# Kernel optimization log

Measured on AMD Instinct MI355X. Metric: run time of the kernel, lower is better.

## Reference

```python
import jax, jax.numpy as jnp
import numpy as np

N, C_IN, C_OUT, T, V = 64, 128, 128, 128, 25
REL = C_IN // 8  # rel_channels = 16


def setup_inputs() -> dict:
    key = jax.random.key(0)
    ks = jax.random.split(key, 12)
    s_in = 1.0 / np.sqrt(C_IN)
    s_rel = 1.0 / np.sqrt(REL)
    return {
        "x": jax.random.normal(ks[0], (N, C_IN, T, V), jnp.float32),
        "A": jax.random.normal(ks[1], (V, V), jnp.float32),
        "alpha": jnp.float32(1.0),
        "W1": jax.random.normal(ks[2], (REL, C_IN), jnp.float32) * s_in,
        "b1": jnp.zeros((REL,), jnp.float32),
        "W2": jax.random.normal(ks[3], (REL, C_IN), jnp.float32) * s_in,
        "b2": jnp.zeros((REL,), jnp.float32),
        "W3": jax.random.normal(ks[4], (C_OUT, C_IN), jnp.float32) * s_in,
        "b3": jnp.zeros((C_OUT,), jnp.float32),
        "W4": jax.random.normal(ks[5], (C_OUT, REL), jnp.float32) * s_rel,
        "b4": jnp.zeros((C_OUT,), jnp.float32),
    }


def reference(x, A, alpha, W1, b1, W2, b2, W3, b3, W4, b4):
    # conv1(x).mean(-2) and conv2(x).mean(-2): 1x1 conv is linear, so mean over
    # T commutes with it -> compute mean first to avoid an (N,REL,T,V) temp.
    xm = x.mean(axis=2)                                        # (N, C, V)
    x1 = jnp.einsum('rc,ncv->nrv', W1, xm) + b1[None, :, None]  # (N, R, V)
    x2 = jnp.einsum('rc,ncv->nrv', W2, xm) + b2[None, :, None]  # (N, R, V)
    x3 = jnp.einsum('oc,nctv->notv', W3, x) + b3[None, :, None, None]  # (N,O,T,V)
    # tanh of broadcasted pairwise difference: (N, R, V, V)
    d = jnp.tanh(x1[:, :, :, None] - x2[:, :, None, :])
    # conv4 (1x1 over channel dim) -> learned per-channel adjacency
    adj = jnp.einsum('or,nrvu->novu', W4, d) + b4[None, :, None, None]
    adj = adj * alpha + A[None, None, :, :]                    # (N, O, V, V)
    return jnp.einsum('ncvu,nctv->nctu', adj, x3)              # (N, O, T, V)
```

## Files before the change

### kernel.cpp

```cpp
#include <hip/hip_runtime.h>


#define NB   64
#define CIN  128
#define COUT 128
#define TT   128
#define VV   25
#define REL  16

#define JT 25
#define KT 4
#define CT 8
#define XF_BYTES (JT * KT * 1024)
#define W3F_OFF  XF_BYTES
#define LDS_BYTES (XF_BYTES + CT * KT * 1024)
#define X3_STRIDE 1040

typedef __attribute__((ext_vector_type(8))) short bf16x8;
typedef __attribute__((ext_vector_type(4))) float f32x4;

__device__ inline short f2bf(float f) {
    unsigned u = __float_as_uint(f);
    u += 0x7fff + ((u >> 16) & 1);
    return (short)(u >> 16);
}

__launch_bounds__(256)
__global__ void k_mean(const float* __restrict__ x, float* __restrict__ xm) {
    __shared__ float tile[4 * 3200];
    int tid = threadIdx.x;
    int c0 = blockIdx.x * 4, n = blockIdx.y;
    const float* src = x + ((size_t)n * CIN + c0) * 3200;
    for (int i = tid; i < 3200; i += 256)
        *reinterpret_cast<float4*>(&tile[i * 4]) =
            *reinterpret_cast<const float4*>(src + (size_t)i * 4);
    __syncthreads();
    if (tid < 100) {
        int cl = tid / 25, v = tid - cl * 25;
        const float* r = &tile[cl * 3200 + v];
        float s = 0.f;
#pragma unroll
        for (int t = 0; t < TT; ++t) s += r[t * 25];
        xm[((size_t)n * CIN + c0 + cl) * 25 + v] = s * (1.0f / TT);
    }
}

__global__ void k_adj(const float* __restrict__ xm,
                      const float* __restrict__ A, const float* __restrict__ alphap,
                      const float* __restrict__ W1, const float* __restrict__ b1,
                      const float* __restrict__ W2, const float* __restrict__ b2,
                      const float* __restrict__ W4, const float* __restrict__ b4,
                      char* __restrict__ adjT) {
    __shared__ char adjS[32 * 2048];
    __shared__ float xms[CIN * VV];
    __shared__ float W1s[REL * CIN];
    __shared__ float W2s[REL * CIN];
    __shared__ float x1s[REL * VV];
    __shared__ float x2s[REL * VV];
    __shared__ float W4s[32 * REL];
    __shared__ float b4s[32];

    int tid = threadIdx.x;
    int n = blockIdx.x;
    int o0 = blockIdx.y * 32;

    for (int i = tid; i < 16384; i += 256) reinterpret_cast<float*>(adjS)[i] = 0.f;
    for (int i = tid; i < CIN * VV; i += 256) xms[i] = xm[(size_t)n * CIN * VV + i];
    for (int i = tid; i < REL * CIN; i += 256) { W1s[i] = W1[i]; W2s[i] = W2[i]; }
    for (int i = tid; i < 32 * REL; i += 256) W4s[i] = W4[o0 * REL + i];
    if (tid < 32) b4s[tid] = b4[o0 + tid];
    __syncthreads();

    for (int task = tid; task < 2 * REL * VV; task += 256) {
        int rv = task % (REL * VV);
        int which = task / (REL * VV);
        int r = rv / VV, v = rv % VV;
        const float* Ws = which ? W2s : W1s;
        float s = 0.f;
#pragma unroll 8
        for (int c = 0; c < CIN; ++c) s = fmaf(Ws[r * CIN + c], xms[c * VV + v], s);
        s += which ? b2[r] : b1[r];
        (which ? x2s : x1s)[rv] = s;
    }
    __syncthreads();

    float alpha = alphap[0];
    for (int p = tid; p < VV * VV; p += 256) {
        int v = p / VV, u = p % VV;
        float d[REL];
#pragma unroll
        for (int r = 0; r < REL; ++r) d[r] = tanhf(x1s[r * VV + v] - x2s[r * VV + u]);
        float Avu = A[v * VV + u];
        int off = (u >> 4) * 1024 + (((u & 15) + 16 * (v >> 3)) * 16) + (v & 7) * 2;
        for (int oo = 0; oo < 32; ++oo) {
            float s = 0.f;
#pragma unroll
            for (int r = 0; r < REL; ++r) s = fmaf(W4s[oo * REL + r], d[r], s);
            float val = alpha * (s + b4s[oo]) + Avu;
            *(short*)(adjS + oo * 2048 + off) = f2bf(val);
        }
    }
    __syncthreads();

    float4* dst = reinterpret_cast<float4*>(adjT + (size_t)(n * COUT + o0) * 2048);
    const float4* src = reinterpret_cast<const float4*>(adjS);
    for (int i = tid; i < 4096; i += 256) dst[i] = src[i];
}

__launch_bounds__(512)
__global__ void k_main(const float* __restrict__ x, const float* __restrict__ W3,
                       const float* __restrict__ b3, const char* __restrict__ adjT,
                       float* __restrict__ out) {
    __shared__ __align__(16) char lds[LDS_BYTES];

    int tid = threadIdx.x;
    int tb = blockIdx.x, n = blockIdx.y;
    int lane = tid & 63, w = tid >> 6;
    int g = lane >> 4, lr = lane & 15;

    const float* xb = x + (size_t)n * (CIN * TT * VV) + tb * (16 * VV);

    bf16x8 xr[13];
#pragma unroll
    for (int q = 0; q < 13; ++q) {
        int chunk = tid + q * 512;
        if (chunk < JT * KT * 64) {
            int l = chunk & 63;
            int frag = chunk >> 6;
            int kt = frag / JT, jt = frag % JT;
            int j = jt * 16 + (l & 15);
            int kb = kt * 32 + 8 * (l >> 4);
            const float* p = xb + (size_t)kb * (TT * VV) + j;
#pragma unroll
            for (int b = 0; b < 8; ++b) xr[q][b] = f2bf(p[(size_t)b * (TT * VV)]);
        }
    }
#pragma unroll
    for (int q = 0; q < 13; ++q) {
        int chunk = tid + q * 512;
        if (chunk < JT * KT * 64)
            *reinterpret_cast<bf16x8*>(lds + (size_t)chunk * 16) = xr[q];
    }
#pragma unroll
    for (int q = 0; q < 4; ++q) {
        int chunk = tid + q * 512;
        int l = chunk & 63;
        int frag = chunk >> 6;
        int ct = frag >> 2, kt = frag & 3;
        int c = ct * 16 + (l & 15);
        int kb = kt * 32 + 8 * (l >> 4);
        const float4 f0 = *reinterpret_cast<const float4*>(&W3[(size_t)c * CIN + kb]);
        const float4 f1 = *reinterpret_cast<const float4*>(&W3[(size_t)c * CIN + kb + 4]);
        bf16x8 vv;
        vv[0] = f2bf(f0.x); vv[1] = f2bf(f0.y); vv[2] = f2bf(f0.z); vv[3] = f2bf(f0.w);
        vv[4] = f2bf(f1.x); vv[5] = f2bf(f1.y); vv[6] = f2bf(f1.z); vv[7] = f2bf(f1.w);
        *reinterpret_cast<bf16x8*>(lds + W3F_OFF + (size_t)chunk * 16) = vv;
    }
    __syncthreads();

    f32x4 acc[JT];
#pragma unroll
    for (int jt = 0; jt < JT; ++jt) acc[jt] = f32x4{0.f, 0.f, 0.f, 0.f};
#pragma unroll
    for (int kt = 0; kt < KT; ++kt) {
        bf16x8 a = *reinterpret_cast<const bf16x8*>(lds + W3F_OFF + ((w * 4 + kt) * 64 + lane) * 16);
#pragma unroll
        for (int jt = 0; jt < JT; ++jt) {
            bf16x8 bx = *reinterpret_cast<const bf16x8*>(lds + ((kt * JT + jt) * 64 + lane) * 16);
            acc[jt] = __builtin_amdgcn_mfma_f32_16x16x32_bf16(a, bx, acc[jt], 0, 0, 0);
        }
    }
    __syncthreads();

    int cbase = w * 16 + 4 * g;
    float bv[4];
#pragma unroll
    for (int r = 0; r < 4; ++r) bv[r] = b3[cbase + r];
#pragma unroll
    for (int jt = 0; jt < JT; ++jt) {
        int j = jt * 16 + lr;
        int t = j / 25, v = j - t * 25;
        int off = (t + 16 * (v >> 3)) * 16 + (v & 7) * 2;
#pragma unroll
        for (int r = 0; r < 4; ++r) {
            float val = acc[jt][r] + bv[r];
            *(short*)(lds + (size_t)(cbase + r) * X3_STRIDE + off) = f2bf(val);
        }
    }
    for (int z = lane; z < 16 * 16 * 7; z += 64) {
        int c = 16 * w + z / 112;
        int rem = z % 112;
        int t = rem / 7, qq = rem % 7;
        *(short*)(lds + (size_t)c * X3_STRIDE + (t + 48) * 16 + 2 + qq * 2) = 0;
    }

    const char* adjTb = adjT + (size_t)(n * COUT) * 2048;
    int t0 = tb * 16;
    for (int cc = 0; cc < 16; ++cc) {
        int c = w * 16 + cc;
        bf16x8 a = *reinterpret_cast<const bf16x8*>(lds + (size_t)c * X3_STRIDE + lane * 16);
        const bf16x8* bp = reinterpret_cast<const bf16x8*>(adjTb + (size_t)c * 2048);
        bf16x8 b0 = bp[lane];
        bf16x8 b1 = bp[64 + lane];
        f32x4 z = {0.f, 0.f, 0.f, 0.f};
        f32x4 d0 = __builtin_amdgcn_mfma_f32_16x16x32_bf16(a, b0, z, 0, 0, 0);
        f32x4 d1 = __builtin_amdgcn_mfma_f32_16x16x32_bf16(a, b1, z, 0, 0, 0);
        float* ob = out + ((size_t)(n * COUT + c) * TT + t0) * VV;
#pragma unroll
        for (int r = 0; r < 4; ++r) {
            int t = 4 * g + r;
            ob[(size_t)t * VV + lr] = d0[r];
            if (lr < 9) ob[(size_t)t * VV + 16 + lr] = d1[r];
        }
    }
}

extern "C" void kernel_launch(void* const* d_in, const int* in_sizes, int n_in,
                              void* d_out, int out_size, void* d_ws, size_t ws_size,
                              hipStream_t stream) {
    const float* x     = (const float*)d_in[0];
    const float* A     = (const float*)d_in[1];
    const float* alpha = (const float*)d_in[2];
    const float* W1    = (const float*)d_in[3];
    const float* b1    = (const float*)d_in[4];
    const float* W2    = (const float*)d_in[5];
    const float* b2    = (const float*)d_in[6];
    const float* W3    = (const float*)d_in[7];
    const float* b3    = (const float*)d_in[8];
    const float* W4    = (const float*)d_in[9];
    const float* b4    = (const float*)d_in[10];
    float* out = (float*)d_out;

    float* xm  = (float*)d_ws;
    char* adjT = (char*)d_ws + 819200;

    k_mean<<<dim3(CIN / 4, NB), 256, 0, stream>>>(x, xm);
    k_adj<<<dim3(NB, 4), 256, 0, stream>>>(xm, A, alpha, W1, b1, W2, b2, W4, b4, adjT);
    k_main<<<dim3(TT / 16, NB), 512, 0, stream>>>(x, W3, b3, adjT, out);
}
```

Baseline: 118.8 us.

## Pre-pack W3 to bf16 fragments once and shrink k_main LDS footprint

W3 is converted to bf16 MFMA fragment layout once inside k_adj (block n==0) and stored in workspace, so k_main reads the fragments straight from global memory instead of converting W3 in every block. The x tile is now staged in two K-halves through a 51 KB LDS buffer rather than a single ~134 KB one, and the x3 scratch is processed per wave in four slices. Launch bounds request 4 waves per SIMD. Together these aim to raise occupancy and cut redundant conversion work. The cost is extra barriers, more global loads of A fragments, and likely register pressure from the 25 accumulators under the tighter bound.

Result: slower. 183.3 us (+54.3%).

```diff
diff --git a/kernel.cpp b/kernel.cpp
--- a/kernel.cpp
+++ b/kernel.cpp
@@ -9,12 +9,9 @@
 #define REL  16
 
 #define JT 25
-#define KT 4
-#define CT 8
-#define XF_BYTES (JT * KT * 1024)
-#define W3F_OFF  XF_BYTES
-#define LDS_BYTES (XF_BYTES + CT * KT * 1024)
-#define X3_STRIDE 1040
+#define XH_BYTES 51200
+#define SCR_STRIDE 1040
+#define SCR_WAVE   (4 * SCR_STRIDE)
 
 typedef __attribute__((ext_vector_type(8))) short bf16x8;
 typedef __attribute__((ext_vector_type(4))) float f32x4;
@@ -50,6 +47,7 @@
                       const float* __restrict__ W1, const float* __restrict__ b1,
                       const float* __restrict__ W2, const float* __restrict__ b2,
                       const float* __restrict__ W4, const float* __restrict__ b4,
+                      const float* __restrict__ W3, char* __restrict__ W3f,
                       char* __restrict__ adjT) {
     __shared__ char adjS[32 * 2048];
     __shared__ float xms[CIN * VV];
@@ -63,6 +61,24 @@
     int tid = threadIdx.x;
     int n = blockIdx.x;
     int o0 = blockIdx.y * 32;
+
+    if (n == 0) {
+#pragma unroll
+        for (int pass = 0; pass < 2; ++pass) {
+            int chunk = blockIdx.y * 512 + pass * 256 + tid;
+            int l = chunk & 63;
+            int frag = chunk >> 6;
+            int ct = frag >> 2, kt = frag & 3;
+            int c = ct * 16 + (l & 15);
+            int kb = kt * 32 + 8 * (l >> 4);
+            const float4 f0 = *reinterpret_cast<const float4*>(&W3[(size_t)c * CIN + kb]);
+            const float4 f1 = *reinterpret_cast<const float4*>(&W3[(size_t)c * CIN + kb + 4]);
+            bf16x8 vv;
+            vv[0] = f2bf(f0.x); vv[1] = f2bf(f0.y); vv[2] = f2bf(f0.z); vv[3] = f2bf(f0.w);
+            vv[4] = f2bf(f1.x); vv[5] = f2bf(f1.y); vv[6] = f2bf(f1.z); vv[7] = f2bf(f1.w);
+            *reinterpret_cast<bf16x8*>(W3f + (size_t)chunk * 16) = vv;
+        }
+    }
 
     for (int i = tid; i < 16384; i += 256) reinterpret_cast<float*>(adjS)[i] = 0.f;
     for (int i = tid; i < CIN * VV; i += 256) xms[i] = xm[(size_t)n * CIN * VV + i];
@@ -107,11 +123,11 @@
     for (int i = tid; i < 4096; i += 256) dst[i] = src[i];
 }
 
-__launch_bounds__(512)
-__global__ void k_main(const float* __restrict__ x, const float* __restrict__ W3,
+__launch_bounds__(512, 4)
+__global__ void k_main(const float* __restrict__ x, const char* __restrict__ W3f,
                        const float* __restrict__ b3, const char* __restrict__ adjT,
                        float* __restrict__ out) {
-    __shared__ __align__(16) char lds[LDS_BYTES];
+    __shared__ __align__(16) char lds[XH_BYTES];
 
     int tid = threadIdx.x;
     int tb = blockIdx.x, n = blockIdx.y;
@@ -120,97 +136,84 @@
 
     const float* xb = x + (size_t)n * (CIN * TT * VV) + tb * (16 * VV);
 
-    bf16x8 xr[13];
-#pragma unroll
-    for (int q = 0; q < 13; ++q) {
-        int chunk = tid + q * 512;
-        if (chunk < JT * KT * 64) {
-            int l = chunk & 63;
-            int frag = chunk >> 6;
-            int kt = frag / JT, jt = frag % JT;
-            int j = jt * 16 + (l & 15);
-            int kb = kt * 32 + 8 * (l >> 4);
-            const float* p = xb + (size_t)kb * (TT * VV) + j;
-#pragma unroll
-            for (int b = 0; b < 8; ++b) xr[q][b] = f2bf(p[(size_t)b * (TT * VV)]);
-        }
-    }
-#pragma unroll
-    for (int q = 0; q < 13; ++q) {
-        int chunk = tid + q * 512;
-        if (chunk < JT * KT * 64)
-            *reinterpret_cast<bf16x8*>(lds + (size_t)chunk * 16) = xr[q];
-    }
-#pragma unroll
-    for (int q = 0; q < 4; ++q) {
-        int chunk = tid + q * 512;
-        int l = chunk & 63;
-        int frag = chunk >> 6;
-        int ct = frag >> 2, kt = frag & 3;
-        int c = ct * 16 + (l & 15);
-        int kb = kt * 32 + 8 * (l >> 4);
-        const float4 f0 = *reinterpret_cast<const float4*>(&W3[(size_t)c * CIN + kb]);
-        const float4 f1 = *reinterpret_cast<const float4*>(&W3[(size_t)c * CIN + kb + 4]);
-        bf16x8 vv;
-        vv[0] = f2bf(f0.x); vv[1] = f2bf(f0.y); vv[2] = f2bf(f0.z); vv[3] = f2bf(f0.w);
-        vv[4] = f2bf(f1.x); vv[5] = f2bf(f1.y); vv[6] = f2bf(f1.z); vv[7] = f2bf(f1.w);
-        *reinterpret_cast<bf16x8*>(lds + W3F_OFF + (size_t)chunk * 16) = vv;
-    }
-    __syncthreads();
-
     f32x4 acc[JT];
 #pragma unroll
     for (int jt = 0; jt < JT; ++jt) acc[jt] = f32x4{0.f, 0.f, 0.f, 0.f};
-#pragma unroll
-    for (int kt = 0; kt < KT; ++kt) {
-        bf16x8 a = *reinterpret_cast<const bf16x8*>(lds + W3F_OFF + ((w * 4 + kt) * 64 + lane) * 16);
-#pragma unroll
-        for (int jt = 0; jt < JT; ++jt) {
-            bf16x8 bx = *reinterpret_cast<const bf16x8*>(lds + ((kt * JT + jt) * 64 + lane) * 16);
-            acc[jt] = __builtin_amdgcn_mfma_f32_16x16x32_bf16(a, bx, acc[jt], 0, 0, 0);
-        }
-    }
-    __syncthreads();
-
-    int cbase = w * 16 + 4 * g;
-    float bv[4];
-#pragma unroll
-    for (int r = 0; r < 4; ++r) bv[r] = b3[cbase + r];
-#pragma unroll
-    for (int jt = 0; jt < JT; ++jt) {
-        int j = jt * 16 + lr;
-        int t = j / 25, v = j - t * 25;
-        int off = (t + 16 * (v >> 3)) * 16 + (v & 7) * 2;
-#pragma unroll
-        for (int r = 0; r < 4; ++r) {
-            float val = acc[jt][r] + bv[r];
-            *(short*)(lds + (size_t)(cbase + r) * X3_STRIDE + off) = f2bf(val);
-        }
-    }
-    for (int z = lane; z < 16 * 16 * 7; z += 64) {
-        int c = 16 * w + z / 112;
-        int rem = z % 112;
-        int t = rem / 7, qq = rem % 7;
-        *(short*)(lds + (size_t)c * X3_STRIDE + (t + 48) * 16 + 2 + qq * 2) = 0;
+
+#pragma unroll
+    for (int h = 0; h < 2; ++h) {
+#pragma unroll
+        for (int q = 0; q < 7; ++q) {
+            int chunk = tid + q * 512;
+            if (chunk < 3200) {
+                int l = chunk & 63;
+                int frag = chunk >> 6;
+                int kk = (frag >= JT) ? 1 : 0;
+                int jt = frag - kk * JT;
+                int j = jt * 16 + (l & 15);
+                int kb = (h * 2 + kk) * 32 + 8 * (l >> 4);
+                const float* p = xb + (size_t)kb * (TT * VV) + j;
+                bf16x8 v;
+#pragma unroll
+                for (int b = 0; b < 8; ++b) v[b] = f2bf(p[(size_t)b * (TT * VV)]);
+                *reinterpret_cast<bf16x8*>(lds + (size_t)chunk * 16) = v;
+            }
+        }
+        __syncthreads();
+
+#pragma unroll
+        for (int kk = 0; kk < 2; ++kk) {
+            int kt = h * 2 + kk;
+            bf16x8 a = *reinterpret_cast<const bf16x8*>(
+                W3f + (size_t)((w * 4 + kt) * 64 + lane) * 16);
+#pragma unroll
+            for (int jt = 0; jt < JT; ++jt) {
+                bf16x8 bx = *reinterpret_cast<const bf16x8*>(
+                    lds + (size_t)((kk * JT + jt) * 64 + lane) * 16);
+                acc[jt] = __builtin_amdgcn_mfma_f32_16x16x32_bf16(a, bx, acc[jt], 0, 0, 0);
+            }
+        }
+        __syncthreads();
     }
 
     const char* adjTb = adjT + (size_t)(n * COUT) * 2048;
     int t0 = tb * 16;
-    for (int cc = 0; cc < 16; ++cc) {
-        int c = w * 16 + cc;
-        bf16x8 a = *reinterpret_cast<const bf16x8*>(lds + (size_t)c * X3_STRIDE + lane * 16);
-        const bf16x8* bp = reinterpret_cast<const bf16x8*>(adjTb + (size_t)c * 2048);
-        bf16x8 b0 = bp[lane];
-        bf16x8 b1 = bp[64 + lane];
-        f32x4 z = {0.f, 0.f, 0.f, 0.f};
-        f32x4 d0 = __builtin_amdgcn_mfma_f32_16x16x32_bf16(a, b0, z, 0, 0, 0);
-        f32x4 d1 = __builtin_amdgcn_mfma_f32_16x16x32_bf16(a, b1, z, 0, 0, 0);
-        float* ob = out + ((size_t)(n * COUT + c) * TT + t0) * VV;
-#pragma unroll
-        for (int r = 0; r < 4; ++r) {
-            int t = 4 * g + r;
-            ob[(size_t)t * VV + lr] = d0[r];
-            if (lr < 9) ob[(size_t)t * VV + 16 + lr] = d1[r];
+    char* scr = lds + w * SCR_WAVE;
+#pragma unroll
+    for (int r = 0; r < 4; ++r) {
+        float bvr = b3[w * 16 + 4 * g + r];
+#pragma unroll
+        for (int jt = 0; jt < JT; ++jt) {
+            int j = jt * 16 + lr;
+            int t = j / 25, v = j - t * 25;
+            int off = (t + 16 * (v >> 3)) * 16 + (v & 7) * 2;
+            *(short*)(scr + g * SCR_STRIDE + off) = f2bf(acc[jt][r] + bvr);
+        }
+#pragma unroll
+        for (int z = 0; z < 7; ++z) {
+            int idx = lane + z * 64;
+            int gg = idx / 112;
+            int rem = idx - gg * 112;
+            int t = rem / 7, qq = rem - t * 7;
+            *(short*)(scr + gg * SCR_STRIDE + (t + 48) * 16 + 2 + qq * 2) = 0;
+        }
+#pragma unroll
+        for (int gg = 0; gg < 4; ++gg) {
+            int c = w * 16 + 4 * gg + r;
+            bf16x8 a = *reinterpret_cast<const bf16x8*>(scr + gg * SCR_STRIDE + lane * 16);
+            const bf16x8* bp = reinterpret_cast<const bf16x8*>(adjTb + (size_t)c * 2048);
+            bf16x8 b0 = bp[lane];
+            bf16x8 b1 = bp[64 + lane];
+            f32x4 z = {0.f, 0.f, 0.f, 0.f};
+            f32x4 d0 = __builtin_amdgcn_mfma_f32_16x16x32_bf16(a, b0, z, 0, 0, 0);
+            f32x4 d1 = __builtin_amdgcn_mfma_f32_16x16x32_bf16(a, b1, z, 0, 0, 0);
+            float* ob = out + ((size_t)(n * COUT + c) * TT + t0) * VV;
+#pragma unroll
+            for (int rr = 0; rr < 4; ++rr) {
+                int t = 4 * g + rr;
+                ob[(size_t)t * VV + lr] = d0[rr];
+                if (lr < 9) ob[(size_t)t * VV + 16 + lr] = d1[rr];
+            }
         }
     }
 }
@@ -233,8 +236,10 @@
 
     float* xm  = (float*)d_ws;
     char* adjT = (char*)d_ws + 819200;
+    char* W3f  = (char*)d_ws + 819200 + 16777216;
 
     k_mean<<<dim3(CIN / 4, NB), 256, 0, stream>>>(x, xm);
-    k_adj<<<dim3(NB, 4), 256, 0, stream>>>(xm, A, alpha, W1, b1, W2, b2, W4, b4, adjT);
-    k_main<<<dim3(TT / 16, NB), 512, 0, stream>>>(x, W3, b3, adjT, out);
-}
+    k_adj<<<dim3(NB, 4), 256, 0, stream>>>(xm, A, alpha, W1, b1, W2, b2, W4, b4,
+                                           W3, W3f, adjT);
+    k_main<<<dim3(TT / 16, NB), 512, 0, stream>>>(x, W3f, b3, adjT, out);
+}
```
